# Performance work log

Hardware: AMD Instinct MI355X
Metric: run time of the kernel (lower is better)

## Reference

```python
import jax, jax.numpy as jnp
import numpy as np

B, T, IN, H, OUT = 128, 256, 128, 1024, 2


def _lstm_cell(x, h, c, Wih, Whh, bih, bhh):
    # x: [B, in], h/c: [B, H]; torch LSTMCell gate order: i, f, g, o
    gates = x @ Wih.T + h @ Whh.T + bih + bhh  # [B, 4H]
    i, f, g, o = jnp.split(gates, 4, axis=-1)
    c_new = jax.nn.sigmoid(f) * c + jax.nn.sigmoid(i) * jnp.tanh(g)
    h_new = jax.nn.sigmoid(o) * jnp.tanh(c_new)
    return h_new, c_new


def setup_inputs() -> dict:
    key = jax.random.key(0)
    ks = jax.random.split(key, 11)
    s0 = 1.0 / np.sqrt(H)
    inp = {
        "x": jax.random.normal(ks[0], (B, T, IN), dtype=jnp.float32),
        # layer 0: input IN -> hidden H
        "W_ih0": jax.random.uniform(ks[1], (4 * H, IN), minval=-s0, maxval=s0, dtype=jnp.float32),
        "W_hh0": jax.random.uniform(ks[2], (4 * H, H), minval=-s0, maxval=s0, dtype=jnp.float32),
        "b_ih0": jax.random.uniform(ks[3], (4 * H,), minval=-s0, maxval=s0, dtype=jnp.float32),
        "b_hh0": jax.random.uniform(ks[4], (4 * H,), minval=-s0, maxval=s0, dtype=jnp.float32),
        # layer 1: hidden H -> hidden H
        "W_ih1": jax.random.uniform(ks[5], (4 * H, H), minval=-s0, maxval=s0, dtype=jnp.float32),
        "W_hh1": jax.random.uniform(ks[6], (4 * H, H), minval=-s0, maxval=s0, dtype=jnp.float32),
        "b_ih1": jax.random.uniform(ks[7], (4 * H,), minval=-s0, maxval=s0, dtype=jnp.float32),
        "b_hh1": jax.random.uniform(ks[8], (4 * H,), minval=-s0, maxval=s0, dtype=jnp.float32),
        # dense head H -> OUT, then tanh (final_act_type)
        "Wd": jax.random.uniform(ks[9], (OUT, H), minval=-s0, maxval=s0, dtype=jnp.float32),
        "bd": jax.random.uniform(ks[10], (OUT,), minval=-s0, maxval=s0, dtype=jnp.float32),
    }
    return inp


def reference(x, W_ih0, W_hh0, b_ih0, b_hh0, W_ih1, W_hh1, b_ih1, b_hh1, Wd, bd):
    b = x.shape[0]
    init = (jnp.zeros((b, H), x.dtype), jnp.zeros((b, H), x.dtype),
            jnp.zeros((b, H), x.dtype), jnp.zeros((b, H), x.dtype))

    def step(carry, x_t):
        h0, c0, h1, c1 = carry
        h0, c0 = _lstm_cell(x_t, h0, c0, W_ih0, W_hh0, b_ih0, b_hh0)
        h1, c1 = _lstm_cell(h0, h1, c1, W_ih1, W_hh1, b_ih1, b_hh1)
        return (h0, c0, h1, c1), None

    (h0, c0, h1, c1), _ = jax.lax.scan(step, init, jnp.swapaxes(x, 0, 1))
    # dropout_rate=0 -> identity; dense + tanh
    return jnp.tanh(h1 @ Wd.T + bd)
```

## Files before the change

### kernel.cpp

```cpp
#include <hip/hip_runtime.h>
#include <hip/hip_fp16.h>
#include <hip/hip_cooperative_groups.h>

namespace cg = cooperative_groups;

typedef _Float16 half8 __attribute__((ext_vector_type(8)));
typedef float floatx4 __attribute__((ext_vector_type(4)));

#define NB 128
#define NT 256
#define NIN 128
#define NH 1024

#define H0_OFF   0u
#define H1_OFF   2097152u
#define PART_OFF 4194304u
#define BAR_OFF  8388608u

#define W0STRIDE 648
#define W1STRIDE 1032
#define GSTRIDE  132
#define LDS_BYTES 141568

__device__ __forceinline__ float sigm(float x) { return 1.0f / (1.0f + __expf(-x)); }
__device__ __forceinline__ float tanh_fast(float x) { return 1.0f - 2.0f / (__expf(2.0f * x) + 1.0f); }

__device__ __forceinline__ void st2_agent(_Float16* p, float v) {
    _Float16 hv = (_Float16)v;
    unsigned short u;
    __builtin_memcpy(&u, &hv, 2);
    __hip_atomic_store((unsigned short*)p, u, __ATOMIC_RELAXED, __HIP_MEMORY_SCOPE_AGENT);
}
__device__ __forceinline__ void st4_agent(float* p, float v) {
    __hip_atomic_store(p, v, __ATOMIC_RELAXED, __HIP_MEMORY_SCOPE_AGENT);
}
__device__ __forceinline__ void ld8_agent(const float* p, float* a, float* b) {
    unsigned long long u = __hip_atomic_load((const unsigned long long*)p,
                                             __ATOMIC_RELAXED, __HIP_MEMORY_SCOPE_AGENT);
    float v2[2];
    __builtin_memcpy(v2, &u, 8);
    *a = v2[0]; *b = v2[1];
}

__device__ __forceinline__ void gbar_arrive(char* bar, unsigned epoch, int wg) {
    unsigned* gcnt = (unsigned*)(bar + (wg & 15) * 256);
    unsigned old = __hip_atomic_fetch_add(gcnt, 1u, __ATOMIC_RELAXED, __HIP_MEMORY_SCOPE_AGENT);
    if (old == epoch * 16u - 1u) {
        unsigned* rcnt = (unsigned*)(bar + 4096);
        unsigned rold = __hip_atomic_fetch_add(rcnt, 1u, __ATOMIC_RELAXED, __HIP_MEMORY_SCOPE_AGENT);
        if (rold == epoch * 16u - 1u) {
            unsigned* flag = (unsigned*)(bar + 4352);
            __hip_atomic_store(flag, epoch, __ATOMIC_RELAXED, __HIP_MEMORY_SCOPE_AGENT);
        }
    }
}
__device__ __forceinline__ void gbar_wait(char* bar, unsigned epoch) {
    unsigned* flag = (unsigned*)(bar + 4352);
    while (__hip_atomic_load(flag, __ATOMIC_RELAXED, __HIP_MEMORY_SCOPE_AGENT) < epoch)
        __builtin_amdgcn_s_sleep(1);
    if ((epoch & 7u) == 0u) {
        __builtin_amdgcn_fence(__ATOMIC_ACQUIRE, "agent");
    } else {
        asm volatile("s_waitcnt vmcnt(0)\n\tbuffer_inv sc0" ::: "memory");
    }
}

__global__ void __launch_bounds__(512, 2)
lstm_persist(const float* __restrict__ x,
             const float* __restrict__ Wih0, const float* __restrict__ Whh0,
             const float* __restrict__ bih0, const float* __restrict__ bhh0,
             const float* __restrict__ Wih1, const float* __restrict__ Whh1,
             const float* __restrict__ bih1, const float* __restrict__ bhh1,
             const float* __restrict__ Wd, const float* __restrict__ bd,
             float* __restrict__ out, char* __restrict__ wsc)
{
    cg::grid_group grid = cg::this_grid();
    const int wg   = blockIdx.x;
    const int g    = wg >> 7;
    const int c    = wg & 127;
    const int tid  = threadIdx.x;
    const int r    = tid >> 6;
    const int lane = tid & 63;
    const int l15  = lane & 15;
    const int quad = lane >> 4;

    _Float16* h0b = (_Float16*)(wsc + H0_OFF);
    _Float16* h1b = (_Float16*)(wsc + H1_OFF);
    char* bar = wsc + BAR_OFF;
    float* part = (float*)(wsc + PART_OFF);
    float* my_part = part + (size_t)(g * 128 + c) * 4096;
    float* pr_part = part + (size_t)((1 - g) * 128 + c) * 4096;
    unsigned* myflag = (unsigned*)(bar + 8192 + c * 128 + g * 4);
    unsigned* prflag = (unsigned*)(bar + 8192 + c * 128 + (1 - g) * 4);

    extern __shared__ char smem[];
    _Float16* w0l = (_Float16*)(smem);
    _Float16* w1l = (_Float16*)(smem + 41472);
    float*    gs0 = (float*)(smem + 107520);
    float*    gs1 = (float*)(smem + 124416);
    float*    bs0 = (float*)(smem + 141312);
    float*    bs1 = (float*)(smem + 141440);

    for (int i = tid; i < 32 * 640; i += 512) {
        int n = i / 640, k = i - n * 640;
        int gcol = ((n >> 3) << 10) + (c << 3) + (n & 7);
        float v = (k < NIN) ? Wih0[gcol * NIN + k] : Whh0[gcol * NH + g * 512 + (k - NIN)];
        w0l[n * W0STRIDE + k] = (_Float16)v;
    }
    for (int i = tid; i < 32 * 1024; i += 512) {
        int n = i >> 10, k = i & 1023;
        int gcol = ((n >> 3) << 10) + (c << 3) + (n & 7);
        float v = (k < 512) ? Wih1[gcol * NH + g * 512 + k] : Whh1[gcol * NH + g * 512 + (k - 512)];
        w1l[n * W1STRIDE + k] = (_Float16)v;
    }
    if (tid < 32) {
        int n = tid;
        int gcol = ((n >> 3) << 10) + (c << 3) + (n & 7);
        bs0[n] = bih0[gcol] + bhh0[gcol];
        bs1[n] = bih1[gcol] + bhh1[gcol];
    }

    {
        const int gtid = wg * 512 + tid;
        const int gsz  = 256 * 512;
        float* hz = (float*)wsc;
        for (int i = gtid; i < 1048576; i += gsz) hz[i] = 0.0f;
        if (wg == 0) {
            if (tid < 18) {
                if (tid < 16)       *(unsigned*)(bar + tid * 256) = 0u;
                else if (tid == 16) *(unsigned*)(bar + 4096) = 0u;
                else                *(unsigned*)(bar + 4352) = 0u;
            }
            for (int i = tid; i < 4096; i += 512) *(unsigned*)(bar + 8192 + i * 4) = 0u;
        }
    }
    __builtin_amdgcn_fence(__ATOMIC_RELEASE, "agent");
    grid.sync();
    __builtin_amdgcn_fence(__ATOMIC_ACQUIRE, "agent");

    float c0 = 0.0f, c1 = 0.0f;
    const int bh_   = tid >> 3;
    const int cl_   = tid & 7;
    const int bact  = g * 64 + bh_;
    const int hcol  = (c << 3) + cl_;
    const int ownhalf = ((r >> 2) == g);
    const int bo_base = r * 16 + quad * 4 - (1 - g) * 64;
    const int nlo = l15 & 7;
    const int nhi = l15 >> 3;

    const _Float16* bw0[2];  const _Float16* bw1i[2];  const _Float16* bw1h[2];  const _Float16* bx[2];
    #pragma unroll
    for (int nt = 0; nt < 2; ++nt) {
        bw0[nt]  = w0l + (nt * 16 + l15) * W0STRIDE + NIN + quad * 8;
        bw1i[nt] = w1l + (nt * 16 + l15) * W1STRIDE + quad * 8;
        bw1h[nt] = bw1i[nt] + 512;
        bx[nt]   = w0l + (nt * 16 + l15) * W0STRIDE + g * 64 + quad * 8;
    }
    const int aoff = (r * 16 + l15) * NH + g * 512 + quad * 8;

    floatx4 accx0 = {0.f,0.f,0.f,0.f}, accx1 = {0.f,0.f,0.f,0.f};

    auto xpart = [&](int t) {
        floatx4 ax0 = {0.f,0.f,0.f,0.f}, ax1 = {0.f,0.f,0.f,0.f};
        const float* xr = x + (size_t)(r * 16 + l15) * (NT * NIN) + t * NIN + g * 64 + quad * 8;
        #pragma unroll
        for (int j = 0; j < 2; ++j) {
            floatx4 f0 = *(const floatx4*)(xr + j * 32);
            floatx4 f1 = *(const floatx4*)(xr + j * 32 + 4);
            half8 a;
            a[0]=(_Float16)f0[0]; a[1]=(_Float16)f0[1]; a[2]=(_Float16)f0[2]; a[3]=(_Float16)f0[3];
            a[4]=(_Float16)f1[0]; a[5]=(_Float16)f1[1]; a[6]=(_Float16)f1[2]; a[7]=(_Float16)f1[3];
            half8 b0 = *(const half8*)(bx[0] + j * 32);
            half8 b1 = *(const half8*)(bx[1] + j * 32);
            ax0 = __builtin_amdgcn_mfma_f32_16x16x32_f16(a, b0, ax0, 0, 0, 0);
            ax1 = __builtin_amdgcn_mfma_f32_16x16x32_f16(a, b1, ax1, 0, 0, 0);
        }
        accx0 = ax0; accx1 = ax1;
    };

    xpart(0);

    for (int p = 0; p <= NT; ++p) {
        const _Float16* arow_h0 = h0b + (size_t)((p + 7) & 7) * (NB * NH) + aoff;
        const _Float16* arow_h1 = h1b + (size_t)((p + 6) & 7) * (NB * NH) + aoff;

        floatx4 acc0[2]  = { accx0, accx1 };
        floatx4 acc1[2]  = { {0.f,0.f,0.f,0.f}, {0.f,0.f,0.f,0.f} };
        floatx4 acc1b[2] = { {0.f,0.f,0.f,0.f}, {0.f,0.f,0.f,0.f} };

        if (p >= 1 && p < NT) {
            #pragma unroll
            for (int jb = 0; jb < 4; ++jb) {
                half8 a0v[4], a1v[4];
                #pragma unroll
                for (int j = 0; j < 4; ++j) a0v[j] = *(const half8*)(arow_h0 + (jb * 4 + j) * 32);
                #pragma unroll
                for (int j = 0; j < 4; ++j) a1v[j] = *(const half8*)(arow_h1 + (jb * 4 + j) * 32);
                #pragma unroll
                for (int j = 0; j < 4; ++j) {
                    #pragma unroll
                    for (int nt = 0; nt < 2; ++nt) {
                        half8 v0 = *(const half8*)(bw0[nt]  + (jb * 4 + j) * 32);
                        half8 v1 = *(const half8*)(bw1i[nt] + (jb * 4 + j) * 32);
                        half8 v2 = *(const half8*)(bw1h[nt] + (jb * 4 + j) * 32);
                        acc0[nt]  = __builtin_amdgcn_mfma_f32_16x16x32_f16(a0v[j], v0, acc0[nt], 0, 0, 0);
                        acc1[nt]  = __builtin_amdgcn_mfma_f32_16x16x32_f16(a0v[j], v1, acc1[nt], 0, 0, 0);
                        acc1b[nt] = __builtin_amdgcn_mfma_f32_16x16x32_f16(a1v[j], v2, acc1b[nt], 0, 0, 0);
                    }
                }
            }
        } else if (p == NT) {
            #pragma unroll
            for (int jb = 0; jb < 4; ++jb) {
                half8 a0v[4], a1v[4];
                #pragma unroll
                for (int j = 0; j < 4; ++j) a0v[j] = *(const half8*)(arow_h0 + (jb * 4 + j) * 32);
                #pragma unroll
                for (int j = 0; j < 4; ++j) a1v[j] = *(const half8*)(arow_h1 + (jb * 4 + j) * 32);
                #pragma unroll
                for (int j = 0; j < 4; ++j) {
                    #pragma unroll
                    for (int nt = 0; nt < 2; ++nt) {
                        half8 v1 = *(const half8*)(bw1i[nt] + (jb * 4 + j) * 32);
                        half8 v2 = *(const half8*)(bw1h[nt] + (jb * 4 + j) * 32);
                        acc1[nt]  = __builtin_amdgcn_mfma_f32_16x16x32_f16(a0v[j], v1, acc1[nt], 0, 0, 0);
                        acc1b[nt] = __builtin_amdgcn_mfma_f32_16x16x32_f16(a1v[j], v2, acc1b[nt], 0, 0, 0);
                    }
                }
            }
        }
        acc1[0] = acc1[0] + acc1b[0];
        acc1[1] = acc1[1] + acc1b[1];

        if (ownhalf) {
            #pragma unroll
            for (int nt = 0; nt < 2; ++nt) {
                if (p < NT)  *(floatx4*)&gs0[(nt * 16 + l15) * GSTRIDE + r * 16 + quad * 4] = acc0[nt];
                if (p >= 1)  *(floatx4*)&gs1[(nt * 16 + l15) * GSTRIDE + r * 16 + quad * 4] = acc1[nt];
            }
        } else {
            #pragma unroll
            for (int nt = 0; nt < 2; ++nt) {
                const int goff = nlo * 4 + 2 * nt + nhi;
                #pragma unroll
                for (int i = 0; i < 4; ++i) {
                    st4_agent(my_part + (bo_base + i) * 32 + goff,        acc0[nt][i]);
                    st4_agent(my_part + 2048 + (bo_base + i) * 32 + goff, acc1[nt][i]);
                }
            }
        }
        __syncthreads();
        if (tid == 0) {
            __hip_atomic_store(myflag, (unsigned)(p + 1), __ATOMIC_RELAXED, __HIP_MEMORY_SCOPE_AGENT);
            while (__hip_atomic_load(prflag, __ATOMIC_RELAXED, __HIP_MEMORY_SCOPE_AGENT) < (unsigned)(p + 1))
                __builtin_amdgcn_s_sleep(1);
        }
        __syncthreads();

        {
            float q0 = 0.f, q1 = 0.f, q2 = 0.f, q3 = 0.f;
            float u0 = 0.f, u1 = 0.f, u2 = 0.f, u3 = 0.f;
            const float* prbase = pr_part + bh_ * 32 + cl_ * 4;
            if (p < NT) {
                ld8_agent(prbase,     &q0, &q1);
                ld8_agent(prbase + 2, &q2, &q3);
            }
            if (p >= 1) {
                ld8_agent(prbase + 2048,     &u0, &u1);
                ld8_agent(prbase + 2048 + 2, &u2, &u3);
            }
            if (p < NT) {
                float gi = gs0[(cl_)      * GSTRIDE + bact] + q0 + bs0[cl_];
                float gf = gs0[(8 + cl_)  * GSTRIDE + bact] + q1 + bs0[8 + cl_];
                float gg = gs0[(16 + cl_) * GSTRIDE + bact] + q2 + bs0[16 + cl_];
                float go = gs0[(24 + cl_) * GSTRIDE + bact] + q3 + bs0[24 + cl_];
                c0 = sigm(gf) * c0 + sigm(gi) * tanh_fast(gg);
                float h = sigm(go) * tanh_fast(c0);
                st2_agent(h0b + (size_t)(p & 7) * (NB * NH) + bact * NH + hcol, h);
            }
            if (p >= 1) {
                float gi = gs1[(cl_)      * GSTRIDE + bact] + u0 + bs1[cl_];
                float gf = gs1[(8 + cl_)  * GSTRIDE + bact] + u1 + bs1[8 + cl_];
                float gg = gs1[(16 + cl_) * GSTRIDE + bact] + u2 + bs1[16 + cl_];
                float go = gs1[(24 + cl_) * GSTRIDE + bact] + u3 + bs1[24 + cl_];
                c1 = sigm(gf) * c1 + sigm(gi) * tanh_fast(gg);
                float h = sigm(go) * tanh_fast(c1);
                st2_agent(h1b + (size_t)((p + 7) & 7) * (NB * NH) + bact * NH + hcol, h);
            }
        }

        __syncthreads();
        if (tid == 0) gbar_arrive(bar, (unsigned)(p + 1), wg);
        if (p + 1 < NT) xpart(p + 1);
        if (tid == 0) gbar_wait(bar, (unsigned)(p + 1));
        __syncthreads();
    }

    if (wg < NB) {
        const _Float16* hrow = h1b + (size_t)7 * (NB * NH) + wg * NH;
        float hk0 = (float)hrow[tid * 2];
        float hk1 = (float)hrow[tid * 2 + 1];
        float p0 = hk0 * Wd[tid * 2] + hk1 * Wd[tid * 2 + 1];
        float p1 = hk0 * Wd[NH + tid * 2] + hk1 * Wd[NH + tid * 2 + 1];
        #pragma unroll
        for (int off = 32; off; off >>= 1) {
            p0 += __shfl_down(p0, off);
            p1 += __shfl_down(p1, off);
        }
        float* red = gs0;
        if (lane == 0) { red[r * 2] = p0; red[r * 2 + 1] = p1; }
        __syncthreads();
        if (tid < 2) {
            float s = bd[tid];
            #pragma unroll
            for (int w = 0; w < 8; ++w) s += red[w * 2 + tid];
            out[wg * 2 + tid] = tanhf(s);
        }
    }
}

extern "C" void kernel_launch(void* const* d_in, const int* in_sizes, int n_in,
                              void* d_out, int out_size, void* d_ws, size_t ws_size,
                              hipStream_t stream) {
    const float* x    = (const float*)d_in[0];
    const float* Wih0 = (const float*)d_in[1];
    const float* Whh0 = (const float*)d_in[2];
    const float* bih0 = (const float*)d_in[3];
    const float* bhh0 = (const float*)d_in[4];
    const float* Wih1 = (const float*)d_in[5];
    const float* Whh1 = (const float*)d_in[6];
    const float* bih1 = (const float*)d_in[7];
    const float* bhh1 = (const float*)d_in[8];
    const float* Wd   = (const float*)d_in[9];
    const float* bd   = (const float*)d_in[10];
    float* out = (float*)d_out;
    char* ws = (char*)d_ws;

    hipFuncSetAttribute((const void*)lstm_persist,
                        hipFuncAttributeMaxDynamicSharedMemorySize, LDS_BYTES);

    void* kargs[] = { &x, &Wih0, &Whh0, &bih0, &bhh0, &Wih1, &Whh1, &bih1, &bhh1,
                      &Wd, &bd, &out, &ws };
    hipLaunchCooperativeKernel((void*)lstm_persist, dim3(256), dim3(512),
                               kargs, LDS_BYTES, stream);
}
```

Before: 3.397 ms.

## Repartition work into 4-way K split with 64 hidden columns per group

Changes the grid decomposition from a 2-way split of the reduction dimension with 128 column groups to a 4-way split with 64 column groups of 16 hidden units each. Each workgroup now computes 64 gate columns over a quarter of K, exchanges partial sums with three peer workgroups via global memory using 8-byte stores, and waits on three flags. The h ring buffers shrink from 8 to 4 slots. This raises MFMA work per weight load and reduces the number of distinct column tiles, at the cost of more cross-workgroup partial-sum traffic and synchronization per step.

After: 3.726 ms. +9.7%, slower.

```diff
diff --git a/kernel.cpp b/kernel.cpp
--- a/kernel.cpp
+++ b/kernel.cpp
@@ -13,14 +13,14 @@
 #define NH 1024
 
 #define H0_OFF   0u
-#define H1_OFF   2097152u
-#define PART_OFF 4194304u
-#define BAR_OFF  8388608u
-
-#define W0STRIDE 648
-#define W1STRIDE 1032
-#define GSTRIDE  132
-#define LDS_BYTES 141568
+#define H1_OFF   1048576u
+#define PART_OFF 2097152u
+#define BAR_OFF  14680064u
+
+#define W0STRIDE 328
+#define W1STRIDE 520
+#define GSTRIDE  36
+#define LDS_BYTES 127488
 
 __device__ __forceinline__ float sigm(float x) { return 1.0f / (1.0f + __expf(-x)); }
 __device__ __forceinline__ float tanh_fast(float x) { return 1.0f - 2.0f / (__expf(2.0f * x) + 1.0f); }
@@ -31,8 +31,11 @@
     __builtin_memcpy(&u, &hv, 2);
     __hip_atomic_store((unsigned short*)p, u, __ATOMIC_RELAXED, __HIP_MEMORY_SCOPE_AGENT);
 }
-__device__ __forceinline__ void st4_agent(float* p, float v) {
-    __hip_atomic_store(p, v, __ATOMIC_RELAXED, __HIP_MEMORY_SCOPE_AGENT);
+__device__ __forceinline__ void st8_agent(float* p, float a, float b) {
+    float v2[2] = { a, b };
+    unsigned long long u;
+    __builtin_memcpy(&u, v2, 8);
+    __hip_atomic_store((unsigned long long*)p, u, __ATOMIC_RELAXED, __HIP_MEMORY_SCOPE_AGENT);
 }
 __device__ __forceinline__ void ld8_agent(const float* p, float* a, float* b) {
     unsigned long long u = __hip_atomic_load((const unsigned long long*)p,
@@ -58,7 +61,7 @@
     unsigned* flag = (unsigned*)(bar + 4352);
     while (__hip_atomic_load(flag, __ATOMIC_RELAXED, __HIP_MEMORY_SCOPE_AGENT) < epoch)
         __builtin_amdgcn_s_sleep(1);
-    if ((epoch & 7u) == 0u) {
+    if ((epoch & 3u) == 0u) {
         __builtin_amdgcn_fence(__ATOMIC_ACQUIRE, "agent");
     } else {
         asm volatile("s_waitcnt vmcnt(0)\n\tbuffer_inv sc0" ::: "memory");
@@ -76,8 +79,8 @@
 {
     cg::grid_group grid = cg::this_grid();
     const int wg   = blockIdx.x;
-    const int g    = wg >> 7;
-    const int c    = wg & 127;
+    const int g    = wg >> 6;
+    const int c    = wg & 63;
     const int tid  = threadIdx.x;
     const int r    = tid >> 6;
     const int lane = tid & 63;
@@ -88,34 +91,33 @@
     _Float16* h1b = (_Float16*)(wsc + H1_OFF);
     char* bar = wsc + BAR_OFF;
     float* part = (float*)(wsc + PART_OFF);
-    float* my_part = part + (size_t)(g * 128 + c) * 4096;
-    float* pr_part = part + (size_t)((1 - g) * 128 + c) * 4096;
-    unsigned* myflag = (unsigned*)(bar + 8192 + c * 128 + g * 4);
-    unsigned* prflag = (unsigned*)(bar + 8192 + c * 128 + (1 - g) * 4);
+    unsigned* myflag = (unsigned*)(bar + 8192 + (g * 64 + c) * 64);
 
     extern __shared__ char smem[];
     _Float16* w0l = (_Float16*)(smem);
-    _Float16* w1l = (_Float16*)(smem + 41472);
-    float*    gs0 = (float*)(smem + 107520);
-    float*    gs1 = (float*)(smem + 124416);
-    float*    bs0 = (float*)(smem + 141312);
-    float*    bs1 = (float*)(smem + 141440);
-
-    for (int i = tid; i < 32 * 640; i += 512) {
-        int n = i / 640, k = i - n * 640;
-        int gcol = ((n >> 3) << 10) + (c << 3) + (n & 7);
-        float v = (k < NIN) ? Wih0[gcol * NIN + k] : Whh0[gcol * NH + g * 512 + (k - NIN)];
+    _Float16* w1l = (_Float16*)(smem + 41984);
+    float*    gs0 = (float*)(smem + 108544);
+    float*    gs1 = (float*)(smem + 117760);
+    float*    bs0 = (float*)(smem + 126976);
+    float*    bs1 = (float*)(smem + 127232);
+
+    for (int i = tid; i < 64 * 288; i += 512) {
+        int n = i / 288, k = i - n * 288;
+        int gcol = ((n >> 4) << 10) + (c << 4) + (n & 15);
+        float v = (k < 32) ? Wih0[gcol * NIN + g * 32 + k]
+                           : Whh0[gcol * NH + g * 256 + (k - 32)];
         w0l[n * W0STRIDE + k] = (_Float16)v;
     }
-    for (int i = tid; i < 32 * 1024; i += 512) {
-        int n = i >> 10, k = i & 1023;
-        int gcol = ((n >> 3) << 10) + (c << 3) + (n & 7);
-        float v = (k < 512) ? Wih1[gcol * NH + g * 512 + k] : Whh1[gcol * NH + g * 512 + (k - 512)];
+    for (int i = tid; i < 64 * 512; i += 512) {
+        int n = i >> 9, k = i & 511;
+        int gcol = ((n >> 4) << 10) + (c << 4) + (n & 15);
+        float v = (k < 256) ? Wih1[gcol * NH + g * 256 + k]
+                            : Whh1[gcol * NH + g * 256 + (k - 256)];
         w1l[n * W1STRIDE + k] = (_Float16)v;
     }
-    if (tid < 32) {
+    if (tid < 64) {
         int n = tid;
-        int gcol = ((n >> 3) << 10) + (c << 3) + (n & 7);
+        int gcol = ((n >> 4) << 10) + (c << 4) + (n & 15);
         bs0[n] = bih0[gcol] + bhh0[gcol];
         bs1[n] = bih1[gcol] + bhh1[gcol];
     }
@@ -124,7 +126,7 @@
         const int gtid = wg * 512 + tid;
         const int gsz  = 256 * 512;
         float* hz = (float*)wsc;
-        for (int i = gtid; i < 1048576; i += gsz) hz[i] = 0.0f;
+        for (int i = gtid; i < 524288; i += gsz) hz[i] = 0.0f;
         if (wg == 0) {
             if (tid < 18) {
                 if (tid < 16)       *(unsigned*)(bar + tid * 256) = 0u;
@@ -139,58 +141,54 @@
     __builtin_amdgcn_fence(__ATOMIC_ACQUIRE, "agent");
 
     float c0 = 0.0f, c1 = 0.0f;
-    const int bh_   = tid >> 3;
-    const int cl_   = tid & 7;
-    const int bact  = g * 64 + bh_;
-    const int hcol  = (c << 3) + cl_;
-    const int ownhalf = ((r >> 2) == g);
-    const int bo_base = r * 16 + quad * 4 - (1 - g) * 64;
-    const int nlo = l15 & 7;
-    const int nhi = l15 >> 3;
-
-    const _Float16* bw0[2];  const _Float16* bw1i[2];  const _Float16* bw1h[2];  const _Float16* bx[2];
+    const int bh_   = tid >> 4;
+    const int cl_   = tid & 15;
+    const int bact  = g * 32 + bh_;
+    const int hcol  = (c << 4) + cl_;
+    const int q_    = r >> 1;
+    const int ownq  = (q_ == g);
+    const int bo_base = (r & 1) * 16 + quad * 4;
+
+    const _Float16* bw0[4];  const _Float16* bw1i[4];  const _Float16* bw1h[4];  const _Float16* bx[4];
     #pragma unroll
-    for (int nt = 0; nt < 2; ++nt) {
-        bw0[nt]  = w0l + (nt * 16 + l15) * W0STRIDE + NIN + quad * 8;
+    for (int nt = 0; nt < 4; ++nt) {
+        bw0[nt]  = w0l + (nt * 16 + l15) * W0STRIDE + 32 + quad * 8;
         bw1i[nt] = w1l + (nt * 16 + l15) * W1STRIDE + quad * 8;
-        bw1h[nt] = bw1i[nt] + 512;
-        bx[nt]   = w0l + (nt * 16 + l15) * W0STRIDE + g * 64 + quad * 8;
-    }
-    const int aoff = (r * 16 + l15) * NH + g * 512 + quad * 8;
-
-    floatx4 accx0 = {0.f,0.f,0.f,0.f}, accx1 = {0.f,0.f,0.f,0.f};
+        bw1h[nt] = bw1i[nt] + 256;
+        bx[nt]   = w0l + (nt * 16 + l15) * W0STRIDE + quad * 8;
+    }
+    const int aoff = (r * 16 + l15) * NH + g * 256 + quad * 8;
+
+    floatx4 accx[4] = { {0,0,0,0}, {0,0,0,0}, {0,0,0,0}, {0,0,0,0} };
 
     auto xpart = [&](int t) {
-        floatx4 ax0 = {0.f,0.f,0.f,0.f}, ax1 = {0.f,0.f,0.f,0.f};
-        const float* xr = x + (size_t)(r * 16 + l15) * (NT * NIN) + t * NIN + g * 64 + quad * 8;
+        const float* xr = x + (size_t)(r * 16 + l15) * (NT * NIN) + t * NIN + g * 32 + quad * 8;
+        floatx4 f0 = *(const floatx4*)(xr);
+        floatx4 f1 = *(const floatx4*)(xr + 4);
+        half8 a;
+        a[0]=(_Float16)f0[0]; a[1]=(_Float16)f0[1]; a[2]=(_Float16)f0[2]; a[3]=(_Float16)f0[3];
+        a[4]=(_Float16)f1[0]; a[5]=(_Float16)f1[1]; a[6]=(_Float16)f1[2]; a[7]=(_Float16)f1[3];
         #pragma unroll
-        for (int j = 0; j < 2; ++j) {
-            floatx4 f0 = *(const floatx4*)(xr + j * 32);
-            floatx4 f1 = *(const floatx4*)(xr + j * 32 + 4);
-            half8 a;
-            a[0]=(_Float16)f0[0]; a[1]=(_Float16)f0[1]; a[2]=(_Float16)f0[2]; a[3]=(_Float16)f0[3];
-            a[4]=(_Float16)f1[0]; a[5]=(_Float16)f1[1]; a[6]=(_Float16)f1[2]; a[7]=(_Float16)f1[3];
-            half8 b0 = *(const half8*)(bx[0] + j * 32);
-            half8 b1 = *(const half8*)(bx[1] + j * 32);
-            ax0 = __builtin_amdgcn_mfma_f32_16x16x32_f16(a, b0, ax0, 0, 0, 0);
-            ax1 = __builtin_amdgcn_mfma_f32_16x16x32_f16(a, b1, ax1, 0, 0, 0);
-        }
-        accx0 = ax0; accx1 = ax1;
+        for (int nt = 0; nt < 4; ++nt) {
+            floatx4 z = {0.f, 0.f, 0.f, 0.f};
+            half8 b = *(const half8*)(bx[nt]);
+            accx[nt] = __builtin_amdgcn_mfma_f32_16x16x32_f16(a, b, z, 0, 0, 0);
+        }
     };
 
     xpart(0);
 
     for (int p = 0; p <= NT; ++p) {
-        const _Float16* arow_h0 = h0b + (size_t)((p + 7) & 7) * (NB * NH) + aoff;
-        const _Float16* arow_h1 = h1b + (size_t)((p + 6) & 7) * (NB * NH) + aoff;
-
-        floatx4 acc0[2]  = { accx0, accx1 };
-        floatx4 acc1[2]  = { {0.f,0.f,0.f,0.f}, {0.f,0.f,0.f,0.f} };
-        floatx4 acc1b[2] = { {0.f,0.f,0.f,0.f}, {0.f,0.f,0.f,0.f} };
+        const _Float16* arow_h0 = h0b + (size_t)((p + 3) & 3) * (NB * NH) + aoff;
+        const _Float16* arow_h1 = h1b + (size_t)((p + 2) & 3) * (NB * NH) + aoff;
+
+        floatx4 acc0[4]  = { accx[0], accx[1], accx[2], accx[3] };
+        floatx4 acc1[4]  = { {0,0,0,0}, {0,0,0,0}, {0,0,0,0}, {0,0,0,0} };
+        floatx4 acc1b[4] = { {0,0,0,0}, {0,0,0,0}, {0,0,0,0}, {0,0,0,0} };
 
         if (p >= 1 && p < NT) {
             #pragma unroll
-            for (int jb = 0; jb < 4; ++jb) {
+            for (int jb = 0; jb < 2; ++jb) {
                 half8 a0v[4], a1v[4];
                 #pragma unroll
                 for (int j = 0; j < 4; ++j) a0v[j] = *(const half8*)(arow_h0 + (jb * 4 + j) * 32);
@@ -199,7 +197,7 @@
                 #pragma unroll
                 for (int j = 0; j < 4; ++j) {
                     #pragma unroll
-                    for (int nt = 0; nt < 2; ++nt) {
+                    for (int nt = 0; nt < 4; ++nt) {
                         half8 v0 = *(const half8*)(bw0[nt]  + (jb * 4 + j) * 32);
                         half8 v1 = *(const half8*)(bw1i[nt] + (jb * 4 + j) * 32);
                         half8 v2 = *(const half8*)(bw1h[nt] + (jb * 4 + j) * 32);
@@ -211,7 +209,7 @@
             }
         } else if (p == NT) {
             #pragma unroll
-            for (int jb = 0; jb < 4; ++jb) {
+            for (int jb = 0; jb < 2; ++jb) {
                 half8 a0v[4], a1v[4];
                 #pragma unroll
                 for (int j = 0; j < 4; ++j) a0v[j] = *(const half8*)(arow_h0 + (jb * 4 + j) * 32);
@@ -220,7 +218,7 @@
                 #pragma unroll
                 for (int j = 0; j < 4; ++j) {
                     #pragma unroll
-                    for (int nt = 0; nt < 2; ++nt) {
+                    for (int nt = 0; nt < 4; ++nt) {
                         half8 v1 = *(const half8*)(bw1i[nt] + (jb * 4 + j) * 32);
                         half8 v2 = *(const half8*)(bw1h[nt] + (jb * 4 + j) * 32);
                         acc1[nt]  = __builtin_amdgcn_mfma_f32_16x16x32_f16(a0v[j], v1, acc1[nt], 0, 0, 0);
@@ -229,63 +227,65 @@
                 }
             }
         }
-        acc1[0] = acc1[0] + acc1b[0];
-        acc1[1] = acc1[1] + acc1b[1];
-
-        if (ownhalf) {
-            #pragma unroll
-            for (int nt = 0; nt < 2; ++nt) {
-                if (p < NT)  *(floatx4*)&gs0[(nt * 16 + l15) * GSTRIDE + r * 16 + quad * 4] = acc0[nt];
-                if (p >= 1)  *(floatx4*)&gs1[(nt * 16 + l15) * GSTRIDE + r * 16 + quad * 4] = acc1[nt];
+        #pragma unroll
+        for (int nt = 0; nt < 4; ++nt) acc1[nt] = acc1[nt] + acc1b[nt];
+
+        if (ownq) {
+            #pragma unroll
+            for (int nt = 0; nt < 4; ++nt) {
+                *(floatx4*)&gs0[(nt * 16 + l15) * GSTRIDE + bo_base] = acc0[nt];
+                *(floatx4*)&gs1[(nt * 16 + l15) * GSTRIDE + bo_base] = acc1[nt];
             }
         } else {
-            #pragma unroll
-            for (int nt = 0; nt < 2; ++nt) {
-                const int goff = nlo * 4 + 2 * nt + nhi;
-                #pragma unroll
-                for (int i = 0; i < 4; ++i) {
-                    st4_agent(my_part + (bo_base + i) * 32 + goff,        acc0[nt][i]);
-                    st4_agent(my_part + 2048 + (bo_base + i) * 32 + goff, acc1[nt][i]);
-                }
-            }
-        }
-        __syncthreads();
-        if (tid == 0) {
+            const int slot = g - (g > q_ ? 1 : 0);
+            float* dst = part + ((size_t)(q_ * 64 + c) * 3 + slot) * 4096;
+            #pragma unroll
+            for (int i = 0; i < 4; ++i) {
+                int off = (bo_base + i) * 64 + l15 * 4;
+                st8_agent(dst + off,            acc0[0][i], acc0[1][i]);
+                st8_agent(dst + off + 2,        acc0[2][i], acc0[3][i]);
+                st8_agent(dst + 2048 + off,     acc1[0][i], acc1[1][i]);
+                st8_agent(dst + 2048 + off + 2, acc1[2][i], acc1[3][i]);
+            }
+        }
+        __syncthreads();
+        if (tid == 0)
             __hip_atomic_store(myflag, (unsigned)(p + 1), __ATOMIC_RELAXED, __HIP_MEMORY_SCOPE_AGENT);
-            while (__hip_atomic_load(prflag, __ATOMIC_RELAXED, __HIP_MEMORY_SCOPE_AGENT) < (unsigned)(p + 1))
+        if (tid < 3) {
+            int sg = tid + (tid >= g ? 1 : 0);
+            unsigned* f = (unsigned*)(bar + 8192 + (sg * 64 + c) * 64);
+            while (__hip_atomic_load(f, __ATOMIC_RELAXED, __HIP_MEMORY_SCOPE_AGENT) < (unsigned)(p + 1))
                 __builtin_amdgcn_s_sleep(1);
         }
         __syncthreads();
 
         {
-            float q0 = 0.f, q1 = 0.f, q2 = 0.f, q3 = 0.f;
-            float u0 = 0.f, u1 = 0.f, u2 = 0.f, u3 = 0.f;
-            const float* prbase = pr_part + bh_ * 32 + cl_ * 4;
+            const float* sb = part + (size_t)(g * 64 + c) * 3 * 4096 + bh_ * 64 + cl_ * 4;
+            float pa0, pa1, pa2, pa3, pb0, pb1, pb2, pb3, pc0, pc1, pc2, pc3;
+            float ua0, ua1, ua2, ua3, ub0, ub1, ub2, ub3, uc0, uc1, uc2, uc3;
+            ld8_agent(sb,                 &pa0, &pa1); ld8_agent(sb + 2,            &pa2, &pa3);
+            ld8_agent(sb + 4096,          &pb0, &pb1); ld8_agent(sb + 4096 + 2,     &pb2, &pb3);
+            ld8_agent(sb + 8192,          &pc0, &pc1); ld8_agent(sb + 8192 + 2,     &pc2, &pc3);
+            ld8_agent(sb + 2048,          &ua0, &ua1); ld8_agent(sb + 2048 + 2,     &ua2, &ua3);
+            ld8_agent(sb + 4096 + 2048,   &ub0, &ub1); ld8_agent(sb + 4096 + 2050,  &ub2, &ub3);
+            ld8_agent(sb + 8192 + 2048,   &uc0, &uc1); ld8_agent(sb + 8192 + 2050,  &uc2, &uc3);
             if (p < NT) {
-                ld8_agent(prbase,     &q0, &q1);
-                ld8_agent(prbase + 2, &q2, &q3);
-            }
-            if (p >= 1) {
-                ld8_agent(prbase + 2048,     &u0, &u1);
-                ld8_agent(prbase + 2048 + 2, &u2, &u3);
-            }
-            if (p < NT) {
-                float gi = gs0[(cl_)      * GSTRIDE + bact] + q0 + bs0[cl_];
-                float gf = gs0[(8 + cl_)  * GSTRIDE + bact] + q1 + bs0[8 + cl_];
-                float gg = gs0[(16 + cl_) * GSTRIDE + bact] + q2 + bs0[16 + cl_];
-                float go = gs0[(24 + cl_) * GSTRIDE + bact] + q3 + bs0[24 + cl_];
+                float gi = gs0[(cl_)      * GSTRIDE + bh_] + pa0 + pb0 + pc0 + bs0[cl_];
+                float gf = gs0[(16 + cl_) * GSTRIDE + bh_] + pa1 + pb1 + pc1 + bs0[16 + cl_];
+                float gg = gs0[(32 + cl_) * GSTRIDE + bh_] + pa2 + pb2 + pc2 + bs0[32 + cl_];
+                float go = gs0[(48 + cl_) * GSTRIDE + bh_] + pa3 + pb3 + pc3 + bs0[48 + cl_];
                 c0 = sigm(gf) * c0 + sigm(gi) * tanh_fast(gg);
                 float h = sigm(go) * tanh_fast(c0);
-                st2_agent(h0b + (size_t)(p & 7) * (NB * NH) + bact * NH + hcol, h);
+                st2_agent(h0b + (size_t)(p & 3) * (NB * NH) + bact * NH + hcol, h);
             }
             if (p >= 1) {
-                float gi = gs1[(cl_)      * GSTRIDE + bact] + u0 + bs1[cl_];
-                float gf = gs1[(8 + cl_)  * GSTRIDE + bact] + u1 + bs1[8 + cl_];
-                float gg = gs1[(16 + cl_) * GSTRIDE + bact] + u2 + bs1[16 + cl_];
-                float go = gs1[(24 + cl_) * GSTRIDE + bact] + u3 + bs1[24 + cl_];
+                float gi = gs1[(cl_)      * GSTRIDE + bh_] + ua0 + ub0 + uc0 + bs1[cl_];
+                float gf = gs1[(16 + cl_) * GSTRIDE + bh_] + ua1 + ub1 + uc1 + bs1[16 + cl_];
+                float gg = gs1[(32 + cl_) * GSTRIDE + bh_] + ua2 + ub2 + uc2 + bs1[32 + cl_];
+                float go = gs1[(48 + cl_) * GSTRIDE + bh_] + ua3 + ub3 + uc3 + bs1[48 + cl_];
                 c1 = sigm(gf) * c1 + sigm(gi) * tanh_fast(gg);
                 float h = sigm(go) * tanh_fast(c1);
-                st2_agent(h1b + (size_t)((p + 7) & 7) * (NB * NH) + bact * NH + hcol, h);
+                st2_agent(h1b + (size_t)((p + 3) & 3) * (NB * NH) + bact * NH + hcol, h);
             }
         }
 
@@ -297,7 +297,7 @@
     }
 
     if (wg < NB) {
-        const _Float16* hrow = h1b + (size_t)7 * (NB * NH) + wg * NH;
+        const _Float16* hrow = h1b + (size_t)3 * (NB * NH) + wg * NH;
         float hk0 = (float)hrow[tid * 2];
         float hk1 = (float)hrow[tid * 2 + 1];
         float p0 = hk0 * Wd[tid * 2] + hk1 * Wd[tid * 2 + 1];
```
